# Kernel optimization log

Measured on AMD Instinct MI355X. Metric: run time of the kernel, lower is better.

The kernel has to match this reference:

```python
import jax, jax.numpy as jnp
import numpy as np

HEADS = 20


def _sdpa(q, k, v):
    # q: [B,H,Sq,D], k/v: [B,H,Sk,D]
    scale = 1.0 / jnp.sqrt(jnp.asarray(q.shape[-1], q.dtype))
    scores = jnp.einsum('bhqd,bhkd->bhqk', q, k) * scale
    probs = jax.nn.softmax(scores, axis=-1)
    return jnp.einsum('bhqk,bhkd->bhqd', probs, v)


def _split_heads(x, B, H):
    # [B,S,H*D] -> [B,H,S,D]
    S = x.shape[1]
    D = x.shape[2] // H
    return x.reshape(B, S, H, D).transpose(0, 2, 1, 3)


def setup_inputs() -> dict:
    key = jax.random.key(0)
    ks = jax.random.split(key, 10)
    B, S, C = 4, 4096, 1280
    T, Lid, X = 77, 32, 2048
    sc = lambda fan_in: 1.0 / np.sqrt(fan_in)
    return {
        'hidden_states': jax.random.normal(ks[0], (B, S, C), jnp.float32),
        'encoder_hidden_states': jax.random.normal(ks[1], (B, T, X), jnp.float32),
        'id_embedding': jax.random.normal(ks[2], (B, Lid, X), jnp.float32),
        'Wq': jax.random.normal(ks[3], (C, C), jnp.float32) * sc(C),
        'Wk': jax.random.normal(ks[4], (C, X), jnp.float32) * sc(X),
        'Wv': jax.random.normal(ks[5], (C, X), jnp.float32) * sc(X),
        'Wik': jax.random.normal(ks[6], (C, X), jnp.float32) * sc(X),
        'Wiv': jax.random.normal(ks[7], (C, X), jnp.float32) * sc(X),
        'Wo': jax.random.normal(ks[8], (C, C), jnp.float32) * sc(C),
        'bo': jnp.zeros((C,), jnp.float32),
    }


def reference(hidden_states, encoder_hidden_states, id_embedding,
              Wq, Wk, Wv, Wik, Wiv, Wo, bo):
    id_scale = 1.0
    B, S, C = hidden_states.shape
    H = HEADS
    residual = hidden_states

    q = _split_heads(hidden_states @ Wq.T, B, H)              # [B,H,S,D]
    k = _split_heads(encoder_hidden_states @ Wk.T, B, H)      # [B,H,T,D]
    v = _split_heads(encoder_hidden_states @ Wv.T, B, H)

    cross = _sdpa(q, k, v)                                    # [B,H,S,D]

    id_k = _split_heads(id_embedding @ Wik.T, B, H)           # [B,H,Lid,D]
    id_v = _split_heads(id_embedding @ Wiv.T, B, H)
    id_out = _sdpa(q, id_k, id_v)                             # [B,H,S,D]

    combined = cross + id_scale * id_out
    combined = combined.transpose(0, 2, 1, 3).reshape(B, S, C)

    out = combined @ Wo.T + bo
    out = out + residual  # residual_connection=True, rescale_output_factor=1.0
    return out
```

## Files before the change

### kernel.cpp

```cpp
#include <hip/hip_runtime.h>

typedef short short8 __attribute__((ext_vector_type(8)));
typedef unsigned short ushort8 __attribute__((ext_vector_type(8)));
typedef float float4v __attribute__((ext_vector_type(4)));

__device__ __forceinline__ unsigned short f2bf(float f) {
    union { float f; unsigned u; } v; v.f = f;
    unsigned r = v.u + 0x7fffu + ((v.u >> 16) & 1u);
    return (unsigned short)(r >> 16);
}

__device__ __forceinline__ void async_copy16(const void* g, void* l) {
    __builtin_amdgcn_global_load_lds(
        (__attribute__((address_space(1))) void*)g,
        (__attribute__((address_space(3))) void*)l,
        16, 0, 0);
}

__global__ __launch_bounds__(256) void cast_bf16_kernel(
        const float* __restrict__ in, unsigned short* __restrict__ out, int n) {
    int i4 = (blockIdx.x * 256 + threadIdx.x) * 4;
    if (i4 < n) {
        float4 f = *(const float4*)(in + i4);
        ushort4 u;
        u.x = f2bf(f.x); u.y = f2bf(f.y); u.z = f2bf(f.z); u.w = f2bf(f.w);
        *(ushort4*)(out + i4) = u;
    }
}

__global__ __launch_bounds__(256) void cast_enc_pad_kernel(
        const float* __restrict__ in, unsigned short* __restrict__ out) {
    int i4 = blockIdx.x * 256 + threadIdx.x;
    if (i4 < 4 * 77 * 2048 / 4) {
        const int per_b = 77 * 2048 / 4;
        int b = i4 / per_b;
        int rem = i4 - b * per_b;
        float4 f = *(const float4*)(in + (size_t)i4 * 4);
        ushort4 u;
        u.x = f2bf(f.x); u.y = f2bf(f.y); u.z = f2bf(f.z); u.w = f2bf(f.w);
        *(ushort4*)(out + ((size_t)b * (96 * 2048 / 4) + rem) * 4) = u;
    }
}

struct CastBatch {
    const float* src[8];
    unsigned short* dst[8];
    int n[8];
};
__global__ __launch_bounds__(256) void cast_batch_kernel(CastBatch cb) {
    const int t = blockIdx.y;
    const int n = cb.n[t];
    int i4 = (blockIdx.x * 256 + threadIdx.x) * 4;
    if (i4 < n) {
        float4 f = *(const float4*)(cb.src[t] + i4);
        ushort4 u;
        u.x = f2bf(f.x); u.y = f2bf(f.y); u.z = f2bf(f.z); u.w = f2bf(f.w);
        *(ushort4*)(cb.dst[t] + i4) = u;
    }
}

template<int EPI>
__device__ __forceinline__ void gemm_core(
        const unsigned short* __restrict__ A,
        const unsigned short* __restrict__ B,
        float* __restrict__ Cf,
        unsigned short* __restrict__ Cb,
        const float* __restrict__ bias,
        const float* __restrict__ resid,
        int Mclamp, int N, int K, int bm, int bn) {
    __shared__ unsigned short As[128 * 64];
    __shared__ unsigned short Bs[128 * 64];

    const int tid  = threadIdx.x;
    const int lane = tid & 63;
    const int wave = tid >> 6;
    const int wm   = (wave >> 1) * 64;
    const int wn   = (wave & 1) * 64;
    const int lr   = lane & 15;
    const int lq   = lane >> 4;

    float4v acc[4][4] = {};

    const unsigned short* aptr[4];
    const unsigned short* bptr[4];
    #pragma unroll
    for (int r = 0; r < 4; ++r) {
        const int linear = r * 256 + tid;
        const int row = linear >> 3;
        const int c = (linear & 7) ^ (row & 7);
        int ar = bm + row; if (ar >= Mclamp) ar = Mclamp - 1;
        aptr[r] = A + (size_t)ar * K + c * 8;
        bptr[r] = B + (size_t)(bn + row) * K + c * 8;
    }

    for (int ks = 0; ks < K; ks += 64) {
        #pragma unroll
        for (int r = 0; r < 4; ++r) {
            async_copy16(aptr[r] + ks, (char*)As + (size_t)(r * 256 + tid) * 16);
            async_copy16(bptr[r] + ks, (char*)Bs + (size_t)(r * 256 + tid) * 16);
        }
        __syncthreads();

        #pragma unroll
        for (int kw = 0; kw < 2; ++kw) {
            short8 af[4], bfr[4];
            #pragma unroll
            for (int i = 0; i < 4; ++i) {
                const int row = wm + i * 16 + lr;
                af[i] = *(const short8*)(As + row * 64 + (((kw << 2) | lq) ^ (row & 7)) * 8);
            }
            #pragma unroll
            for (int j = 0; j < 4; ++j) {
                const int row = wn + j * 16 + lr;
                bfr[j] = *(const short8*)(Bs + row * 64 + (((kw << 2) | lq) ^ (row & 7)) * 8);
            }
            #pragma unroll
            for (int i = 0; i < 4; ++i)
                #pragma unroll
                for (int j = 0; j < 4; ++j)
                    acc[i][j] = __builtin_amdgcn_mfma_f32_16x16x32_bf16(
                                    af[i], bfr[j], acc[i][j], 0, 0, 0);
        }
        __syncthreads();
    }

    #pragma unroll
    for (int i = 0; i < 4; ++i) {
        #pragma unroll
        for (int r = 0; r < 4; ++r) {
            const int row = bm + wm + i * 16 + lq * 4 + r;
            const size_t base = (size_t)row * N;
            #pragma unroll
            for (int j = 0; j < 4; ++j) {
                const int col = bn + wn + j * 16 + lr;
                const float v = acc[i][j][r];
                const size_t idx = base + col;
                if (EPI == 2)      Cf[idx] = v + bias[col] + resid[idx];
                else if (EPI == 1) Cb[idx] = f2bf(v);
                else               Cf[idx] = v;
            }
        }
    }
}

template<int EPI>
__global__ __launch_bounds__(256) void gemm_bt_kernel(
        const unsigned short* __restrict__ A,
        const unsigned short* __restrict__ B,
        float* __restrict__ Cf,
        unsigned short* __restrict__ Cb,
        const float* __restrict__ bias,
        const float* __restrict__ resid,
        int Mclamp, int N, int K) {
    gemm_core<EPI>(A, B, Cf, Cb, bias, resid, Mclamp, N, K,
                   blockIdx.x * 128, blockIdx.y * 128);
}

__global__ __launch_bounds__(256) void gemm_kv4_kernel(
        const unsigned short* __restrict__ Aenc,
        const unsigned short* __restrict__ Aid,
        const unsigned short* __restrict__ Wk,
        const unsigned short* __restrict__ Wv,
        const unsigned short* __restrict__ Wik,
        const unsigned short* __restrict__ Wiv,
        unsigned short* __restrict__ Kb, unsigned short* __restrict__ Vb,
        unsigned short* __restrict__ IKb, unsigned short* __restrict__ IVb,
        int N, int K) {
    const int z = blockIdx.z;
    const int bm = blockIdx.x * 128;
    const int Mrows = (z < 2) ? 384 : 128;
    if (bm >= Mrows) return;
    const unsigned short* A = (z < 2) ? Aenc : Aid;
    const unsigned short* B = (z == 0) ? Wk : (z == 1) ? Wv : (z == 2) ? Wik : Wiv;
    unsigned short* C = (z == 0) ? Kb : (z == 1) ? Vb : (z == 2) ? IKb : IVb;
    gemm_core<1>(A, B, nullptr, C, nullptr, nullptr, Mrows, N, K,
                 bm, blockIdx.y * 128);
}

#define VT_STRIDE 136
__global__ __launch_bounds__(256) void attn_mfma_kernel(
        const unsigned short* __restrict__ Q,
        const unsigned short* __restrict__ Kb,
        const unsigned short* __restrict__ Vb,
        const unsigned short* __restrict__ IKb,
        const unsigned short* __restrict__ IVb,
        unsigned short* __restrict__ Cmb) {
    const int b = blockIdx.z;
    const int h = blockIdx.y;
    const int hoff = h * 64;
    const int qbase = blockIdx.x * 64;
    const int tid = threadIdx.x;
    const int lane = tid & 63;
    const int wave = tid >> 6;
    const int l15 = lane & 15;
    const int quad = lane >> 4;

    __shared__ unsigned short Vt[64 * VT_STRIDE];
    __shared__ unsigned short Pl[64 * VT_STRIDE];

    for (int i = tid; i < 96 * 8; i += 256) {
        const int c = i / 96;
        const int key = i - c * 96;
        short8 v = *(const short8*)(Vb + (size_t)(b * 96 + key) * 1280 + hoff + c * 8);
        #pragma unroll
        for (int j = 0; j < 8; ++j)
            Vt[(c * 8 + j) * VT_STRIDE + key] = (unsigned short)v[j];
    }
    {
        const int c = tid >> 5;
        const int key = tid & 31;
        short8 v = *(const short8*)(IVb + (size_t)(b * 32 + key) * 1280 + hoff + c * 8);
        #pragma unroll
        for (int j = 0; j < 8; ++j)
            Vt[(c * 8 + j) * VT_STRIDE + 96 + key] = (unsigned short)v[j];
    }
    __syncthreads();

    const int qrow = b * 4096 + qbase + wave * 16 + l15;
    const unsigned short* qp = Q + (size_t)qrow * 1280 + hoff + quad * 8;
    const short8 aQ0 = *(const short8*)(qp);
    const short8 aQ1 = *(const short8*)(qp + 32);

    const float scale = 0.125f;
    float lC[4] = {0.f, 0.f, 0.f, 0.f};
    float lI[4] = {0.f, 0.f, 0.f, 0.f};

    #pragma unroll
    for (int t = 0; t < 5; ++t) {
        const unsigned short* kp = Kb + (size_t)(b * 96 + t * 16 + l15) * 1280 + hoff + quad * 8;
        const short8 bK0 = *(const short8*)(kp);
        const short8 bK1 = *(const short8*)(kp + 32);
        float4v s = {};
        s = __builtin_amdgcn_mfma_f32_16x16x32_bf16(aQ0, bK0, s, 0, 0, 0);
        s = __builtin_amdgcn_mfma_f32_16x16x32_bf16(aQ1, bK1, s, 0, 0, 0);
        #pragma unroll
        for (int r = 0; r < 4; ++r) {
            float p = __expf(s[r] * scale);
            if (t == 4 && l15 >= 13) p = 0.f;
            lC[r] += p;
            Pl[(wave * 16 + quad * 4 + r) * VT_STRIDE + t * 16 + l15] = f2bf(p);
        }
    }
    #pragma unroll
    for (int r = 0; r < 4; ++r)
        Pl[(wave * 16 + quad * 4 + r) * VT_STRIDE + 80 + l15] = 0;

    #pragma unroll
    for (int t = 0; t < 2; ++t) {
        const unsigned short* kp = IKb + (size_t)(b * 32 + t * 16 + l15) * 1280 + hoff + quad * 8;
        const short8 bK0 = *(const short8*)(kp);
        const short8 bK1 = *(const short8*)(kp + 32);
        float4v s = {};
        s = __builtin_amdgcn_mfma_f32_16x16x32_bf16(aQ0, bK0, s, 0, 0, 0);
        s = __builtin_amdgcn_mfma_f32_16x16x32_bf16(aQ1, bK1, s, 0, 0, 0);
        #pragma unroll
        for (int r = 0; r < 4; ++r) {
            const float p = __expf(s[r] * scale);
            lI[r] += p;
            Pl[(wave * 16 + quad * 4 + r) * VT_STRIDE + 96 + t * 16 + l15] = f2bf(p);
        }
    }

    #pragma unroll
    for (int m = 1; m <= 8; m <<= 1) {
        #pragma unroll
        for (int r = 0; r < 4; ++r) {
            lC[r] += __shfl_xor(lC[r], m);
            lI[r] += __shfl_xor(lI[r], m);
        }
    }
    __syncthreads();

    float4v oC[4] = {};
    float4v oI[4] = {};
    #pragma unroll
    for (int kt = 0; kt < 3; ++kt) {
        const short8 aP = *(const short8*)(Pl + (wave * 16 + l15) * VT_STRIDE + kt * 32 + quad * 8);
        #pragma unroll
        for (int td = 0; td < 4; ++td) {
            const short8 bV = *(const short8*)(Vt + (td * 16 + l15) * VT_STRIDE + kt * 32 + quad * 8);
            oC[td] = __builtin_amdgcn_mfma_f32_16x16x32_bf16(aP, bV, oC[td], 0, 0, 0);
        }
    }
    {
        const short8 aP = *(const short8*)(Pl + (wave * 16 + l15) * VT_STRIDE + 96 + quad * 8);
        #pragma unroll
        for (int td = 0; td < 4; ++td) {
            const short8 bV = *(const short8*)(Vt + (td * 16 + l15) * VT_STRIDE + 96 + quad * 8);
            oI[td] = __builtin_amdgcn_mfma_f32_16x16x32_bf16(aP, bV, oI[td], 0, 0, 0);
        }
    }

    float rc[4], ri[4];
    #pragma unroll
    for (int r = 0; r < 4; ++r) { rc[r] = 1.f / lC[r]; ri[r] = 1.f / lI[r]; }

    #pragma unroll
    for (int td = 0; td < 4; ++td) {
        #pragma unroll
        for (int r = 0; r < 4; ++r) {
            const int row = b * 4096 + qbase + wave * 16 + quad * 4 + r;
            const int col = hoff + td * 16 + l15;
            Cmb[(size_t)row * 1280 + col] = f2bf(oC[td][r] * rc[r] + oI[td][r] * ri[r]);
        }
    }
}

extern "C" void kernel_launch(void* const* d_in, const int* in_sizes, int n_in,
                              void* d_out, int out_size, void* d_ws, size_t ws_size,
                              hipStream_t stream) {
    const float* hs  = (const float*)d_in[0];
    const float* enc = (const float*)d_in[1];
    const float* idm = (const float*)d_in[2];
    const float* Wq  = (const float*)d_in[3];
    const float* Wk  = (const float*)d_in[4];
    const float* Wv  = (const float*)d_in[5];
    const float* Wik = (const float*)d_in[6];
    const float* Wiv = (const float*)d_in[7];
    const float* Wo  = (const float*)d_in[8];
    const float* bo  = (const float*)d_in[9];
    float* out = (float*)d_out;

    char* ws = (char*)d_ws;
    size_t off = 0;
    auto carve = [&](size_t bytes) {
        char* p = ws + off;
        off += (bytes + 255) & ~(size_t)255;
        return p;
    };

    unsigned short* Xh   = (unsigned short*)carve(16384ULL * 1280 * 2);
    unsigned short* Wq_b = (unsigned short*)carve(1280ULL * 1280 * 2);
    unsigned short* Wk_b = (unsigned short*)carve(1280ULL * 2048 * 2);
    unsigned short* Wv_b = (unsigned short*)carve(1280ULL * 2048 * 2);
    unsigned short* Wik_b= (unsigned short*)carve(1280ULL * 2048 * 2);
    unsigned short* Wiv_b= (unsigned short*)carve(1280ULL * 2048 * 2);
    unsigned short* Wo_b = (unsigned short*)carve(1280ULL * 1280 * 2);
    unsigned short* Encb = (unsigned short*)carve(384ULL * 2048 * 2);
    unsigned short* Idb  = (unsigned short*)carve(128ULL * 2048 * 2);
    unsigned short* Qb   = (unsigned short*)carve(16384ULL * 1280 * 2);
    unsigned short* Kb   = (unsigned short*)carve(384ULL * 1280 * 2);
    unsigned short* Vb   = (unsigned short*)carve(384ULL * 1280 * 2);
    unsigned short* IKb  = (unsigned short*)carve(128ULL * 1280 * 2);
    unsigned short* IVb  = (unsigned short*)carve(128ULL * 1280 * 2);
    (void)ws_size; (void)in_sizes; (void)n_in; (void)out_size;

    cast_bf16_kernel<<<(4 * 4096 * 1280 / 4 + 255) / 256, 256, 0, stream>>>(
        hs, Xh, 4 * 4096 * 1280);
    cast_enc_pad_kernel<<<(4 * 77 * 2048 / 4 + 255) / 256, 256, 0, stream>>>(enc, Encb);

    CastBatch cb;
    cb.src[0] = Wq;  cb.dst[0] = Wq_b;  cb.n[0] = 1280 * 1280;
    cb.src[1] = Wk;  cb.dst[1] = Wk_b;  cb.n[1] = 1280 * 2048;
    cb.src[2] = Wv;  cb.dst[2] = Wv_b;  cb.n[2] = 1280 * 2048;
    cb.src[3] = Wik; cb.dst[3] = Wik_b; cb.n[3] = 1280 * 2048;
    cb.src[4] = Wiv; cb.dst[4] = Wiv_b; cb.n[4] = 1280 * 2048;
    cb.src[5] = Wo;  cb.dst[5] = Wo_b;  cb.n[5] = 1280 * 1280;
    cb.src[6] = idm; cb.dst[6] = Idb;   cb.n[6] = 4 * 32 * 2048;
    cb.src[7] = nullptr; cb.dst[7] = nullptr; cb.n[7] = 0;
    cast_batch_kernel<<<dim3((1280 * 2048 / 4 + 255) / 256, 7), 256, 0, stream>>>(cb);

    gemm_bt_kernel<1><<<dim3(128, 10), 256, 0, stream>>>(
        Xh, Wq_b, nullptr, Qb, nullptr, nullptr, 16384, 1280, 1280);

    gemm_kv4_kernel<<<dim3(3, 10, 4), 256, 0, stream>>>(
        Encb, Idb, Wk_b, Wv_b, Wik_b, Wiv_b, Kb, Vb, IKb, IVb, 1280, 2048);

    attn_mfma_kernel<<<dim3(64, 20, 4), 256, 0, stream>>>(Qb, Kb, Vb, IKb, IVb, Xh);

    gemm_bt_kernel<2><<<dim3(128, 10), 256, 0, stream>>>(
        Xh, Wo_b, out, nullptr, bo, hs, 16384, 1280, 1280);
}
```

Before: 478.3 us.

## Fuse fp32-to-bf16 casts into GEMM tile loads with register-staged prefetch

```diff
diff --git a/kernel.cpp b/kernel.cpp
--- a/kernel.cpp
+++ b/kernel.cpp
@@ -8,13 +8,6 @@
     union { float f; unsigned u; } v; v.f = f;
     unsigned r = v.u + 0x7fffu + ((v.u >> 16) & 1u);
     return (unsigned short)(r >> 16);
-}
-
-__device__ __forceinline__ void async_copy16(const void* g, void* l) {
-    __builtin_amdgcn_global_load_lds(
-        (__attribute__((address_space(1))) void*)g,
-        (__attribute__((address_space(3))) void*)l,
-        16, 0, 0);
 }
 
 __global__ __launch_bounds__(256) void cast_bf16_kernel(
@@ -42,31 +35,12 @@
     }
 }
 
-struct CastBatch {
-    const float* src[8];
-    unsigned short* dst[8];
-    int n[8];
-};
-__global__ __launch_bounds__(256) void cast_batch_kernel(CastBatch cb) {
-    const int t = blockIdx.y;
-    const int n = cb.n[t];
-    int i4 = (blockIdx.x * 256 + threadIdx.x) * 4;
-    if (i4 < n) {
-        float4 f = *(const float4*)(cb.src[t] + i4);
-        ushort4 u;
-        u.x = f2bf(f.x); u.y = f2bf(f.y); u.z = f2bf(f.z); u.w = f2bf(f.w);
-        *(ushort4*)(cb.dst[t] + i4) = u;
-    }
-}
-
-template<int EPI>
+template<int EPI, int AF32, int BF32>
 __device__ __forceinline__ void gemm_core(
-        const unsigned short* __restrict__ A,
-        const unsigned short* __restrict__ B,
-        float* __restrict__ Cf,
-        unsigned short* __restrict__ Cb,
-        const float* __restrict__ bias,
-        const float* __restrict__ resid,
+        const unsigned short* __restrict__ A16, const float* __restrict__ A32,
+        const unsigned short* __restrict__ B16, const float* __restrict__ B32,
+        float* __restrict__ Cf, unsigned short* __restrict__ Cb,
+        const float* __restrict__ bias, const float* __restrict__ resid,
         int Mclamp, int N, int K, int bm, int bn) {
     __shared__ unsigned short As[128 * 64];
     __shared__ unsigned short Bs[128 * 64];
@@ -81,26 +55,70 @@
 
     float4v acc[4][4] = {};
 
-    const unsigned short* aptr[4];
-    const unsigned short* bptr[4];
+    const unsigned short* a16p[4]; const float* a32p[4];
+    const unsigned short* b16p[4]; const float* b32p[4];
+    int ldsOff[4];
     #pragma unroll
     for (int r = 0; r < 4; ++r) {
         const int linear = r * 256 + tid;
         const int row = linear >> 3;
-        const int c = (linear & 7) ^ (row & 7);
+        const int c = linear & 7;
+        ldsOff[r] = row * 64 + (c ^ (row & 7)) * 8;
         int ar = bm + row; if (ar >= Mclamp) ar = Mclamp - 1;
-        aptr[r] = A + (size_t)ar * K + c * 8;
-        bptr[r] = B + (size_t)(bn + row) * K + c * 8;
-    }
-
-    for (int ks = 0; ks < K; ks += 64) {
-        #pragma unroll
-        for (int r = 0; r < 4; ++r) {
-            async_copy16(aptr[r] + ks, (char*)As + (size_t)(r * 256 + tid) * 16);
-            async_copy16(bptr[r] + ks, (char*)Bs + (size_t)(r * 256 + tid) * 16);
-        }
-        __syncthreads();
-
+        if (AF32) a32p[r] = A32 + (size_t)ar * K + c * 8;
+        else      a16p[r] = A16 + (size_t)ar * K + c * 8;
+        if (BF32) b32p[r] = B32 + (size_t)(bn + row) * K + c * 8;
+        else      b16p[r] = B16 + (size_t)(bn + row) * K + c * 8;
+    }
+
+    short8 a16r[4], b16r[4];
+    float4 a32r[4][2], b32r[4][2];
+
+    auto load_tiles = [&](int ks) {
+        #pragma unroll
+        for (int r = 0; r < 4; ++r) {
+            if (AF32) {
+                const float4* p = (const float4*)(a32p[r] + ks);
+                a32r[r][0] = p[0]; a32r[r][1] = p[1];
+            } else {
+                a16r[r] = *(const short8*)(a16p[r] + ks);
+            }
+        }
+        #pragma unroll
+        for (int r = 0; r < 4; ++r) {
+            if (BF32) {
+                const float4* p = (const float4*)(b32p[r] + ks);
+                b32r[r][0] = p[0]; b32r[r][1] = p[1];
+            } else {
+                b16r[r] = *(const short8*)(b16p[r] + ks);
+            }
+        }
+    };
+    auto store_tiles = [&]() {
+        #pragma unroll
+        for (int r = 0; r < 4; ++r) {
+            short8 v;
+            if (AF32) {
+                v[0] = (short)f2bf(a32r[r][0].x); v[1] = (short)f2bf(a32r[r][0].y);
+                v[2] = (short)f2bf(a32r[r][0].z); v[3] = (short)f2bf(a32r[r][0].w);
+                v[4] = (short)f2bf(a32r[r][1].x); v[5] = (short)f2bf(a32r[r][1].y);
+                v[6] = (short)f2bf(a32r[r][1].z); v[7] = (short)f2bf(a32r[r][1].w);
+            } else v = a16r[r];
+            *(short8*)(As + ldsOff[r]) = v;
+        }
+        #pragma unroll
+        for (int r = 0; r < 4; ++r) {
+            short8 v;
+            if (BF32) {
+                v[0] = (short)f2bf(b32r[r][0].x); v[1] = (short)f2bf(b32r[r][0].y);
+                v[2] = (short)f2bf(b32r[r][0].z); v[3] = (short)f2bf(b32r[r][0].w);
+                v[4] = (short)f2bf(b32r[r][1].x); v[5] = (short)f2bf(b32r[r][1].y);
+                v[6] = (short)f2bf(b32r[r][1].z); v[7] = (short)f2bf(b32r[r][1].w);
+            } else v = b16r[r];
+            *(short8*)(Bs + ldsOff[r]) = v;
+        }
+    };
+    auto mfma_phase = [&]() {
         #pragma unroll
         for (int kw = 0; kw < 2; ++kw) {
             short8 af[4], bfr[4];
@@ -121,8 +139,19 @@
                     acc[i][j] = __builtin_amdgcn_mfma_f32_16x16x32_bf16(
                                     af[i], bfr[j], acc[i][j], 0, 0, 0);
         }
+    };
+
+    load_tiles(0);
+    store_tiles();
+    __syncthreads();
+    for (int ks = 64; ks < K; ks += 64) {
+        load_tiles(ks);
+        mfma_phase();
         __syncthreads();
-    }
+        store_tiles();
+        __syncthreads();
+    }
+    mfma_phase();
 
     #pragma unroll
     for (int i = 0; i < 4; ++i) {
@@ -143,26 +172,26 @@
     }
 }
 
-template<int EPI>
-__global__ __launch_bounds__(256) void gemm_bt_kernel(
-        const unsigned short* __restrict__ A,
-        const unsigned short* __restrict__ B,
-        float* __restrict__ Cf,
-        unsigned short* __restrict__ Cb,
-        const float* __restrict__ bias,
-        const float* __restrict__ resid,
-        int Mclamp, int N, int K) {
-    gemm_core<EPI>(A, B, Cf, Cb, bias, resid, Mclamp, N, K,
-                   blockIdx.x * 128, blockIdx.y * 128);
+__global__ __launch_bounds__(256) void gemm_qproj_kernel(
+        const float* __restrict__ A32, const float* __restrict__ B32,
+        unsigned short* __restrict__ Cb, int Mclamp, int N, int K) {
+    gemm_core<1, 1, 1>(nullptr, A32, nullptr, B32, nullptr, Cb, nullptr, nullptr,
+                       Mclamp, N, K, blockIdx.x * 128, blockIdx.y * 128);
+}
+
+__global__ __launch_bounds__(256) void gemm_oproj_kernel(
+        const unsigned short* __restrict__ A16, const float* __restrict__ B32,
+        float* __restrict__ Cf, const float* __restrict__ bias,
+        const float* __restrict__ resid, int Mclamp, int N, int K) {
+    gemm_core<2, 0, 1>(A16, nullptr, nullptr, B32, Cf, nullptr, bias, resid,
+                       Mclamp, N, K, blockIdx.x * 128, blockIdx.y * 128);
 }
 
 __global__ __launch_bounds__(256) void gemm_kv4_kernel(
         const unsigned short* __restrict__ Aenc,
         const unsigned short* __restrict__ Aid,
-        const unsigned short* __restrict__ Wk,
-        const unsigned short* __restrict__ Wv,
-        const unsigned short* __restrict__ Wik,
-        const unsigned short* __restrict__ Wiv,
+        const float* __restrict__ Wk, const float* __restrict__ Wv,
+        const float* __restrict__ Wik, const float* __restrict__ Wiv,
         unsigned short* __restrict__ Kb, unsigned short* __restrict__ Vb,
         unsigned short* __restrict__ IKb, unsigned short* __restrict__ IVb,
         int N, int K) {
@@ -171,10 +200,10 @@
     const int Mrows = (z < 2) ? 384 : 128;
     if (bm >= Mrows) return;
     const unsigned short* A = (z < 2) ? Aenc : Aid;
-    const unsigned short* B = (z == 0) ? Wk : (z == 1) ? Wv : (z == 2) ? Wik : Wiv;
+    const float* B = (z == 0) ? Wk : (z == 1) ? Wv : (z == 2) ? Wik : Wiv;
     unsigned short* C = (z == 0) ? Kb : (z == 1) ? Vb : (z == 2) ? IKb : IVb;
-    gemm_core<1>(A, B, nullptr, C, nullptr, nullptr, Mrows, N, K,
-                 bm, blockIdx.y * 128);
+    gemm_core<1, 0, 1>(A, nullptr, nullptr, B, nullptr, C, nullptr, nullptr,
+                       Mrows, N, K, bm, blockIdx.y * 128);
 }
 
 #define VT_STRIDE 136
@@ -330,12 +359,6 @@
     };
 
     unsigned short* Xh   = (unsigned short*)carve(16384ULL * 1280 * 2);
-    unsigned short* Wq_b = (unsigned short*)carve(1280ULL * 1280 * 2);
-    unsigned short* Wk_b = (unsigned short*)carve(1280ULL * 2048 * 2);
-    unsigned short* Wv_b = (unsigned short*)carve(1280ULL * 2048 * 2);
-    unsigned short* Wik_b= (unsigned short*)carve(1280ULL * 2048 * 2);
-    unsigned short* Wiv_b= (unsigned short*)carve(1280ULL * 2048 * 2);
-    unsigned short* Wo_b = (unsigned short*)carve(1280ULL * 1280 * 2);
     unsigned short* Encb = (unsigned short*)carve(384ULL * 2048 * 2);
     unsigned short* Idb  = (unsigned short*)carve(128ULL * 2048 * 2);
     unsigned short* Qb   = (unsigned short*)carve(16384ULL * 1280 * 2);
@@ -345,29 +368,18 @@
     unsigned short* IVb  = (unsigned short*)carve(128ULL * 1280 * 2);
     (void)ws_size; (void)in_sizes; (void)n_in; (void)out_size;
 
-    cast_bf16_kernel<<<(4 * 4096 * 1280 / 4 + 255) / 256, 256, 0, stream>>>(
-        hs, Xh, 4 * 4096 * 1280);
     cast_enc_pad_kernel<<<(4 * 77 * 2048 / 4 + 255) / 256, 256, 0, stream>>>(enc, Encb);
-
-    CastBatch cb;
-    cb.src[0] = Wq;  cb.dst[0] = Wq_b;  cb.n[0] = 1280 * 1280;
-    cb.src[1] = Wk;  cb.dst[1] = Wk_b;  cb.n[1] = 1280 * 2048;
-    cb.src[2] = Wv;  cb.dst[2] = Wv_b;  cb.n[2] = 1280 * 2048;
-    cb.src[3] = Wik; cb.dst[3] = Wik_b; cb.n[3] = 1280 * 2048;
-    cb.src[4] = Wiv; cb.dst[4] = Wiv_b; cb.n[4] = 1280 * 2048;
-    cb.src[5] = Wo;  cb.dst[5] = Wo_b;  cb.n[5] = 1280 * 1280;
-    cb.src[6] = idm; cb.dst[6] = Idb;   cb.n[6] = 4 * 32 * 2048;
-    cb.src[7] = nullptr; cb.dst[7] = nullptr; cb.n[7] = 0;
-    cast_batch_kernel<<<dim3((1280 * 2048 / 4 + 255) / 256, 7), 256, 0, stream>>>(cb);
-
-    gemm_bt_kernel<1><<<dim3(128, 10), 256, 0, stream>>>(
-        Xh, Wq_b, nullptr, Qb, nullptr, nullptr, 16384, 1280, 1280);
+    cast_bf16_kernel<<<(4 * 32 * 2048 / 4 + 255) / 256, 256, 0, stream>>>(
+        idm, Idb, 4 * 32 * 2048);
+
+    gemm_qproj_kernel<<<dim3(128, 10), 256, 0, stream>>>(
+        hs, Wq, Qb, 16384, 1280, 1280);
 
     gemm_kv4_kernel<<<dim3(3, 10, 4), 256, 0, stream>>>(
-        Encb, Idb, Wk_b, Wv_b, Wik_b, Wiv_b, Kb, Vb, IKb, IVb, 1280, 2048);
+        Encb, Idb, Wk, Wv, Wik, Wiv, Kb, Vb, IKb, IVb, 1280, 2048);
 
     attn_mfma_kernel<<<dim3(64, 20, 4), 256, 0, stream>>>(Qb, Kb, Vb, IKb, IVb, Xh);
 
-    gemm_bt_kernel<2><<<dim3(128, 10), 256, 0, stream>>>(
-        Xh, Wo_b, out, nullptr, bo, hs, 16384, 1280, 1280);
-}
+    gemm_oproj_kernel<<<dim3(128, 10), 256, 0, stream>>>(
+        Xh, Wo, out, bo, hs, 16384, 1280, 1280);
+}
```

Measured after the change: 689.4 us. +44.1%, slower.
